# Performance work log

Hardware: AMD Instinct MI355X
Metric: run time of the kernel (lower is better)

Reference implementation:

```python
import jax, jax.numpy as jnp
import numpy as np
from jax import lax

# 4D convolution (valid padding, stride 1) via XLA's rank-general conv.
# dimension_numbers: N=batch, C=channels, then 4 spatial axes H,W,D,T.
DN = ('NCHWDT', 'OIHWDT', 'NCHWDT')

def conv4d(x, w, b):
    y = lax.conv_general_dilated(x, w, window_strides=(1, 1, 1, 1),
                                 padding='VALID', dimension_numbers=DN)
    return y + b.reshape(1, -1, 1, 1, 1, 1)


def setup_inputs() -> dict:
    key = jax.random.key(0)
    ks = jax.random.split(key, 7)
    B = 128
    x = jax.random.normal(ks[0], (B, 1, 18, 18, 18, 18), dtype=jnp.float32)
    # conv4d(1, 5, 7): weight [out=5, in=1, 7,7,7,7]
    w1 = jax.random.normal(ks[1], (5, 1, 7, 7, 7, 7), dtype=jnp.float32) * 0.02
    b1 = jax.random.normal(ks[2], (5,), dtype=jnp.float32) * 0.02
    # conv4d(5, 10, 7): weight [10, 5, 7,7,7,7]
    w2 = jax.random.normal(ks[3], (10, 5, 7, 7, 7, 7), dtype=jnp.float32) * 0.02
    b2 = jax.random.normal(ks[4], (10,), dtype=jnp.float32) * 0.02
    # Linear(10 * 6**4, 1)
    feat = 10 * 6 ** 4  # 12960
    w_lin = jax.random.normal(ks[5], (1, feat), dtype=jnp.float32) * 0.02
    b_lin = jax.random.normal(ks[6], (1,), dtype=jnp.float32) * 0.02
    return {"x": x, "w1": w1, "b1": b1, "w2": w2, "b2": b2,
            "w_lin": w_lin, "b_lin": b_lin}


def reference(x, w1, b1, w2, b2, w_lin, b_lin):
    # head: conv4d -> ReLU -> conv4d -> ReLU
    h = jax.nn.relu(conv4d(x, w1, b1))          # [B, 5, 12,12,12,12]
    h = jax.nn.relu(conv4d(h, w2, b2))          # [B, 10, 6,6,6,6]
    # out: Flatten -> Dropout(eval: identity) -> Linear -> Sigmoid
    h = h.reshape(h.shape[0], -1)               # [B, 12960]
    logits = h @ w_lin.T + b_lin                 # [B, 1]
    return jax.nn.sigmoid(logits)
```

## Files before the change

### kernel.cpp

```cpp
#include <hip/hip_runtime.h>
#include <math.h>

typedef unsigned u32;
typedef _Float16 f16x8 __attribute__((ext_vector_type(8)));
typedef float    f32x16 __attribute__((ext_vector_type(16)));

static __device__ __forceinline__ u32 pack2(_Float16 a, _Float16 b) {
    union { _Float16 h[2]; u32 u; } v;
    v.h[0] = a; v.h[1] = b;
    return v.u;
}


__global__ __launch_bounds__(256) void pack_A1p(
    const float* __restrict__ w1, _Float16* __restrict__ A1)
{
    int i = blockIdx.x * 256 + threadIdx.x;
    if (i >= 9728) return;
    u32 outv = 0u;
    int kh = i / 1164, r = i % 1164;
    if (kh < 7 && r < 1148) {
        int kw = r / 164, r2 = r % 164;
        if (r2 < 140) {
            int kd = r2 / 20, r3 = r2 % 20;
            int oc = r3 / 4, j2 = r3 % 4;
            int j0 = 2 * j2, j1 = 2 * j2 + 1;
            const float* wb = w1 + oc * 2401 + kh * 343 + kw * 49 + kd * 7;
            _Float16 v0 = (j0 < 7) ? (_Float16)wb[j0] : (_Float16)0.f;
            _Float16 v1 = (j1 < 7) ? (_Float16)wb[j1] : (_Float16)0.f;
            outv = pack2(v0, v1);
        }
    }
    ((u32*)A1)[i] = outv;
}

__global__ __launch_bounds__(256) void pack_A2p(
    const float* __restrict__ w2, _Float16* __restrict__ A2)
{
    int i = blockIdx.x * 256 + threadIdx.x;
    if (i >= 79040) return;
    int ci = i / 15808, r = i % 15808;
    int kh = r / 1976, r2 = r % 1976;
    u32 outv = 0u;
    if (kh < 7 && r2 < 1960) {
        int kw = r2 / 280, r3 = r2 % 280;
        int kd = r3 / 40, r4 = r3 % 40;
        int oc = r4 / 4, j2 = r4 % 4;
        int j0 = 2 * j2, j1 = 2 * j2 + 1;
        const float* wb = w2 + oc * 12005 + ci * 2401 + kh * 343 + kw * 49 + kd * 7;
        _Float16 v0 = (j0 < 7) ? (_Float16)wb[j0] : (_Float16)0.f;
        _Float16 v1 = (j1 < 7) ? (_Float16)wb[j1] : (_Float16)0.f;
        outv = pack2(v0, v1);
    }
    ((u32*)A2)[i] = outv;
}

#define C1_SLAB 9360
#define C1_AOFF 9360
#define C1_LDS  (9360 + 9728)
__global__ __launch_bounds__(256, 2) void conv1_mfma(
    const float* __restrict__ x, const _Float16* __restrict__ A1,
    const float* __restrict__ b1, _Float16* __restrict__ h1)
{
    __shared__ u32 lds[C1_LDS];
    int tid = threadIdx.x;
    int lane = tid & 63;
    int wave = tid >> 6;
    int col = lane & 31;
    int g = lane >> 5;

    int bid = (int)blockIdx.x;
    int lbid = (bid & 7) * 192 + (bid >> 3);
    int OWp = lbid % 3;
    int OH = (lbid / 3) & 3;
    int b = lbid / 12;

    int qn[3], u_[2], od_[2], ot_[2];
    #pragma unroll
    for (int s = 0; s < 2; ++s) {
        int nt = wave + 4 * s;
        int n = nt * 32 + col;
        int u = n / 144, r2 = n % 144;
        int od = r2 / 12, ot = r2 % 12;
        u_[s] = u; od_[s] = od; ot_[s] = ot;
        qn[s] = (u * 36 + od) * 52 + ot * 4;
    }
    {
        int r2 = 112 + col;
        int od = r2 / 12, ot = r2 % 12;
        qn[2] = (36 + od) * 52 + ot * 4;
    }

    f32x16 acc0, acc1, acc2;
    #pragma unroll
    for (int q = 0; q < 16; ++q) { acc0[q] = 0.f; acc1[q] = 0.f; acc2[q] = 0.f; }

    const float* xbase = x + (size_t)b * 104976;
    int w10 = tid / 18, id18 = tid % 18;
    int iw = 4 * OWp + w10;
    bool stager = (tid < 180);

    int mc = (col < 30) ? col : 29;
    int am_dw = mc / 15, am_dh = (mc % 15) / 5, am_oc = mc % 5;
    int jadd = 4 * (col - mc);
    int vlane = 4 * am_oc - 164 * am_dw + jadd;
    int zbase = C1_AOFF + 8312 + vlane;
    bool eLo = (am_dw == 1);
    bool e3  = (am_dw == 1) && (g == 0);
    bool e24 = (am_dw == 0) && (g == 1);
    bool eHi = (am_dw == 0);

    float2 xr[9];
    {
        const uint4* asrc = (const uint4*)A1;
        uint4* adst = (uint4*)(lds + C1_AOFF);
        #pragma unroll
        for (int i = 0; i < 10; ++i) {
            int q = tid + 256 * i;
            if (q < 2432) adst[q] = asrc[q];
        }
        if (stager) {
            const float2* src = (const float2*)(xbase + (3 * OH) * 5832 + iw * 324 + id18 * 18);
            #pragma unroll
            for (int q = 0; q < 9; ++q) xr[q] = src[q];
        }
    }

    for (int se = 0; se < 9; ++se) {
        int kh = se - am_dh;
        int vbase = (kh >= 0 && kh < 7) ? (C1_AOFF + kh * 1164 + vlane) : zbase;

        __syncthreads();
        if (stager) {
            _Float16 h[19];
            #pragma unroll
            for (int q = 0; q < 9; ++q) { h[2*q] = (_Float16)xr[q].x; h[2*q+1] = (_Float16)xr[q].y; }
            h[18] = (_Float16)0.f;
            u32 e[9], o[9];
            #pragma unroll
            for (int q = 0; q < 9; ++q) e[q] = pack2(h[2*q], h[2*q+1]);
            #pragma unroll
            for (int q = 0; q < 9; ++q) o[q] = pack2(h[2*q+1], (q < 8) ? h[2*q+2] : h[18]);
            int base = tid * 52;
            #pragma unroll
            for (int ot = 0; ot < 12; ++ot) {
                uint4 w;
                if ((ot & 1) == 0) { const int q = ot >> 1;   w = (uint4){e[q], e[q+1], e[q+2], e[q+3]}; }
                else               { const int q = (ot-1)>>1; w = (uint4){o[q], o[q+1], o[q+2], o[q+3]}; }
                *(uint4*)(&lds[base + ot * 4]) = w;
            }
        }
        __syncthreads();

        if (se < 8 && stager) {
            const float2* src = (const float2*)(xbase + (3 * OH + se + 1) * 5832 + iw * 324 + id18 * 18);
            #pragma unroll
            for (int q = 0; q < 9; ++q) xr[q] = src[q];
        }

        #pragma unroll
        for (int k2 = 0; k2 < 28; ++k2) {
            const int t0 = 2 * k2, t1 = 2 * k2 + 1;
            const int c0 = ((t0 / 7) * 18 + (t0 % 7)) * 52;
            const int c1 = ((t1 / 7) * 18 + (t1 % 7)) * 52;
            const int ca0 = 164 * (t0 / 7) + 20 * (t0 % 7);
            const int ca1 = 164 * (t1 / 7) + 20 * (t1 % 7);
            int qoff = g ? c1 : c0;
            int ca   = g ? ca1 : ca0;
            int abase;
            if (k2 <= 2)       abase = eLo ? zbase : vbase;
            else if (k2 == 3)  abase = e3  ? zbase : vbase;
            else if (k2 == 24) abase = e24 ? zbase : vbase;
            else if (k2 >= 25) abase = eHi ? zbase : vbase;
            else               abase = vbase;
            f16x8 af = *(const f16x8*)(lds + abase + ca);
            f16x8 bf0 = *(const f16x8*)(lds + qn[0] + qoff);
            f16x8 bf1 = *(const f16x8*)(lds + qn[1] + qoff);
            acc0 = __builtin_amdgcn_mfma_f32_32x32x16_f16(af, bf0, acc0, 0, 0, 0);
            acc1 = __builtin_amdgcn_mfma_f32_32x32x16_f16(af, bf1, acc1, 0, 0, 0);
            if ((k2 & 3) == wave) {
                f16x8 bf2 = *(const f16x8*)(lds + qn[2] + qoff);
                acc2 = __builtin_amdgcn_mfma_f32_32x32x16_f16(af, bf2, acc2, 0, 0, 0);
            }
        }
    }

    #pragma unroll
    for (int s = 0; s < 2; ++s) {
        f32x16 a = (s == 0) ? acc0 : acc1;
        int ow_b = 4 * OWp + 2 * u_[s];
        #pragma unroll
        for (int r = 0; r < 16; ++r) {
            const int m0 = (r & 3) + 8 * (r >> 2);
            const int m1 = m0 + 4;
            const int dw0 = m0 / 15, dh0 = (m0 % 15) / 5, oc0 = m0 % 5;
            const int dw1 = m1 / 15, dh1 = (m1 % 15) / 5, oc1 = m1 % 5;
            if (m1 >= 30 && g) continue;
            int dw = g ? dw1 : dw0;
            int dh = g ? dh1 : dh0;
            int oc = g ? oc1 : oc0;
            float bv = g ? b1[oc1] : b1[oc0];
            float v = fmaxf(a[r] + bv, 0.f);
            h1[(size_t)b * 103680 + oc * 20736 + (3 * OH + dh) * 1728
               + (ow_b + dw) * 144 + od_[s] * 12 + ot_[s]] = (_Float16)v;
        }
    }

    __syncthreads();
    {
        float* fl = (float*)lds;
        #pragma unroll
        for (int r = 0; r < 16; ++r)
            fl[wave * 1024 + r * 64 + lane] = acc2[r];
    }
    __syncthreads();
    {
        const float* fl = (const float*)lds;
        int r2 = 112 + col;
        int od = r2 / 12, ot = r2 % 12;
        int ow_b = 4 * OWp + 2;
        #pragma unroll
        for (int q = 0; q < 4; ++q) {
            int r = wave * 4 + q;
            int m = (r & 3) + 8 * (r >> 2) + 4 * g;
            if (m >= 30) continue;
            float s = fl[r * 64 + lane] + fl[1024 + r * 64 + lane]
                    + fl[2048 + r * 64 + lane] + fl[3072 + r * 64 + lane];
            int dw = m / 15, dh = (m % 15) / 5, oc = m % 5;
            float v = fmaxf(s + b1[oc], 0.f);
            h1[(size_t)b * 103680 + oc * 20736 + (3 * OH + dh) * 1728
               + (ow_b + dw) * 144 + od * 12 + ot] = (_Float16)v;
        }
    }
}

#define C2_SLAB 4032
#define C2_AOFF 4032
#define C2_LDS  (4032 + 15808)
__global__ __launch_bounds__(256, 2) void conv2_mfma(
    const _Float16* __restrict__ h1, const _Float16* __restrict__ A2,
    _Float16* __restrict__ part)
{
    __shared__ u32 lds[C2_LDS];
    int tid = threadIdx.x;
    int lane = tid & 63;
    int wave = tid >> 6;
    int col = lane & 31;
    int g = lane >> 5;

    int bid = (int)blockIdx.x;
    int lbid = (bid & 7) * 160 + (bid >> 3);
    int ci = lbid % 5;
    int OH2 = (lbid / 5) & 1;
    int b = lbid / 10;

    int qn[2], n_[2];
    #pragma unroll
    for (int s = 0; s < 2; ++s) {
        int nt = wave + 4 * s;
        int n = nt * 32 + col;
        n_[s] = n;
        int nc = (n < 216) ? n : 215;
        int ow = nc / 36, rem = nc % 36;
        int od = rem / 6, ot = rem % 6;
        qn[s] = (ow * 12 + od) * 28 + ot * 4;
    }

    f32x16 acc0, acc1;
    #pragma unroll
    for (int q = 0; q < 16; ++q) { acc0[q] = 0.f; acc1[q] = 0.f; }

    const _Float16* hbase = h1 + (size_t)b * 103680 + ci * 20736;
    int iw = tid / 12, id12 = tid % 12;
    bool stager = (tid < 144);

    int mc = (col < 30) ? col : 29;
    int am_dh = mc / 10, am_oc = mc % 10;
    int jadd = 4 * (col - mc);
    int vlane = 4 * am_oc + jadd;
    int zb = C2_AOFF + 13832 + vlane;

    uint2 xr[3];
    {
        const uint4* asrc = (const uint4*)A2 + (size_t)ci * 3952;
        uint4* adst = (uint4*)(lds + C2_AOFF);
        #pragma unroll
        for (int i = 0; i < 16; ++i) {
            int q = tid + 256 * i;
            if (q < 3952) adst[q] = asrc[q];
        }
        if (stager) {
            const uint2* src = (const uint2*)(hbase + (3 * OH2) * 1728 + iw * 144 + id12 * 12);
            #pragma unroll
            for (int q = 0; q < 3; ++q) xr[q] = src[q];
        }
    }

    for (int she = 0; she < 9; ++she) {
        int kh = she - am_dh;
        int vb = (kh >= 0 && kh < 7) ? (C2_AOFF + kh * 1976 + vlane) : zb;

        __syncthreads();
        if (stager) {
            _Float16 h[14];
            *(uint2*)&h[0] = xr[0]; *(uint2*)&h[4] = xr[1]; *(uint2*)&h[8] = xr[2];
            h[12] = (_Float16)0.f;
            u32 e[6], o[6];
            #pragma unroll
            for (int q = 0; q < 6; ++q) e[q] = pack2(h[2*q], h[2*q+1]);
            #pragma unroll
            for (int q = 0; q < 6; ++q) o[q] = pack2(h[2*q+1], (q < 5) ? h[2*q+2] : h[12]);
            int base = tid * 28;
            #pragma unroll
            for (int ot = 0; ot < 6; ++ot) {
                uint4 w;
                if ((ot & 1) == 0) { const int q = ot >> 1;   w = (uint4){e[q], e[q+1], e[q+2], e[q+3]}; }
                else               { const int q = (ot-1)>>1; w = (uint4){o[q], o[q+1], o[q+2], o[q+3]}; }
                *(uint4*)(&lds[base + ot * 4]) = w;
            }
        }
        __syncthreads();

        if (she < 8 && stager) {
            const uint2* src = (const uint2*)(hbase + (3 * OH2 + she + 1) * 1728 + iw * 144 + id12 * 12);
            #pragma unroll
            for (int q = 0; q < 3; ++q) xr[q] = src[q];
        }

        #pragma unroll
        for (int k2 = 0; k2 < 25; ++k2) {
            const int t0 = 2 * k2, t1 = 2 * k2 + 1;
            const int c0 = ((t0 / 7) * 12 + (t0 % 7)) * 28;
            const int c1 = (t1 < 49) ? ((t1 / 7) * 12 + (t1 % 7)) * 28 : 0;
            const int a0 = 280 * (t0 / 7) + 40 * (t0 % 7);
            const int a1 = (t1 < 49) ? (280 * (t1 / 7) + 40 * (t1 % 7)) : 0;
            int qoff = g ? c1 : c0;
            int ca   = g ? a1 : a0;
            int ab = (k2 == 24 && g) ? zb : vb;
            f16x8 af = *(const f16x8*)(lds + ab + ca);
            f16x8 bf0 = *(const f16x8*)(lds + qn[0] + qoff);
            acc0 = __builtin_amdgcn_mfma_f32_32x32x16_f16(af, bf0, acc0, 0, 0, 0);
            if (wave < 3) {
                f16x8 bf1 = *(const f16x8*)(lds + qn[1] + qoff);
                acc1 = __builtin_amdgcn_mfma_f32_32x32x16_f16(af, bf1, acc1, 0, 0, 0);
            }
        }
    }

    #pragma unroll
    for (int s = 0; s < 2; ++s) {
        if (s == 1 && wave >= 3) continue;
        if (n_[s] >= 216) continue;
        f32x16 a = (s == 0) ? acc0 : acc1;
        #pragma unroll
        for (int r = 0; r < 16; ++r) {
            const int m0 = (r & 3) + 8 * (r >> 2);
            const int m1 = m0 + 4;
            const int dh0 = m0 / 10, oc0 = m0 % 10;
            const int dh1 = m1 / 10, oc1 = m1 % 10;
            if (m1 >= 30 && g) continue;
            int dh = g ? dh1 : dh0;
            int oc = g ? oc1 : oc0;
            int oh = 3 * OH2 + dh;
            part[((size_t)(ci * 768 + b * 6 + oh) * 10 + oc) * 216 + n_[s]] = (_Float16)a[r];
        }
    }
}

__global__ __launch_bounds__(256) void out_fused(
    const _Float16* __restrict__ part, const float* __restrict__ b2,
    const float* __restrict__ wl, const float* __restrict__ bl,
    float* __restrict__ out)
{
    int b = blockIdx.x;
    int tid = threadIdx.x;
    float s = 0.f;
    for (int i = tid; i < 12960; i += 256) {
        int oc = i / 1296;
        int rem = i % 1296;
        int oh = rem / 216;
        int n = rem % 216;
        float v = 0.f;
        #pragma unroll
        for (int ci = 0; ci < 5; ++ci)
            v += (float)part[((size_t)(ci * 768 + b * 6 + oh) * 10 + oc) * 216 + n];
        v = fmaxf(v + b2[oc], 0.f);
        s += v * wl[i];
    }
    #pragma unroll
    for (int off = 32; off > 0; off >>= 1)
        s += __shfl_down(s, off, 64);
    __shared__ float wsum[4];
    int wave = tid >> 6;
    if ((tid & 63) == 0) wsum[wave] = s;
    __syncthreads();
    if (tid == 0) {
        float tot = wsum[0] + wsum[1] + wsum[2] + wsum[3] + bl[0];
        out[b] = 1.f / (1.f + expf(-tot));
    }
}

extern "C" void kernel_launch(void* const* d_in, const int* in_sizes, int n_in,
                              void* d_out, int out_size, void* d_ws, size_t ws_size,
                              hipStream_t stream) {
    const float* x  = (const float*)d_in[0];
    const float* w1 = (const float*)d_in[1];
    const float* b1 = (const float*)d_in[2];
    const float* w2 = (const float*)d_in[3];
    const float* b2 = (const float*)d_in[4];
    const float* wl = (const float*)d_in[5];
    const float* bl = (const float*)d_in[6];
    float* out = (float*)d_out;

    _Float16* h1   = (_Float16*)d_ws;
    _Float16* A1   = h1 + 13271040;
    _Float16* A2   = A1 + 129024;
    _Float16* part = A2 + 576000;

    pack_A1p<<<38, 256, 0, stream>>>(w1, A1);
    pack_A2p<<<309, 256, 0, stream>>>(w2, A2);
    conv1_mfma<<<1536, 256, 0, stream>>>(x, A1, b1, h1);
    conv2_mfma<<<1280, 256, 0, stream>>>(h1, A2, part);
    out_fused<<<128, 256, 0, stream>>>(part, b2, wl, bl, out);
}
```

Measured before the change: 232.9 us.

## Balance conv2 MFMA work across waves by splitting remaining N-tiles along K

In conv2_mfma, waves 0-2 previously handled two 32-column N tiles while wave 3 handled one, leaving the load uneven. Now each wave owns one full tile, and the three leftover tiles are split along the reduction (k2) dimension round-robin across all four waves. The partial accumulators are reduced through LDS after a barrier. This evens out MFMA issue per wave, at the cost of three extra accumulator registers sets (register pressure at 2 blocks/SM), an LDS round trip and two extra syncs.

Result: slower. 244.7 us (+5.1%).

```diff
diff --git a/kernel.cpp b/kernel.cpp
--- a/kernel.cpp
+++ b/kernel.cpp
@@ -254,21 +254,25 @@
     int OH2 = (lbid / 5) & 1;
     int b = lbid / 10;
 
-    int qn[2], n_[2];
-    #pragma unroll
-    for (int s = 0; s < 2; ++s) {
-        int nt = wave + 4 * s;
-        int n = nt * 32 + col;
-        n_[s] = n;
+    int qnF, qnR[3];
+    {
+        int n = wave * 32 + col;
+        int ow = n / 36, rem = n % 36;
+        int od = rem / 6, ot = rem % 6;
+        qnF = (ow * 12 + od) * 28 + ot * 4;
+    }
+    #pragma unroll
+    for (int t = 0; t < 3; ++t) {
+        int n = (4 + t) * 32 + col;
         int nc = (n < 216) ? n : 215;
         int ow = nc / 36, rem = nc % 36;
         int od = rem / 6, ot = rem % 6;
-        qn[s] = (ow * 12 + od) * 28 + ot * 4;
-    }
-
-    f32x16 acc0, acc1;
-    #pragma unroll
-    for (int q = 0; q < 16; ++q) { acc0[q] = 0.f; acc1[q] = 0.f; }
+        qnR[t] = (ow * 12 + od) * 28 + ot * 4;
+    }
+
+    f32x16 accF, accR0, accR1, accR2;
+    #pragma unroll
+    for (int q = 0; q < 16; ++q) { accF[q] = 0.f; accR0[q] = 0.f; accR1[q] = 0.f; accR2[q] = 0.f; }
 
     const _Float16* hbase = h1 + (size_t)b * 103680 + ci * 20736;
     int iw = tid / 12, id12 = tid % 12;
@@ -338,31 +342,67 @@
             int ca   = g ? a1 : a0;
             int ab = (k2 == 24 && g) ? zb : vb;
             f16x8 af = *(const f16x8*)(lds + ab + ca);
-            f16x8 bf0 = *(const f16x8*)(lds + qn[0] + qoff);
-            acc0 = __builtin_amdgcn_mfma_f32_32x32x16_f16(af, bf0, acc0, 0, 0, 0);
-            if (wave < 3) {
-                f16x8 bf1 = *(const f16x8*)(lds + qn[1] + qoff);
-                acc1 = __builtin_amdgcn_mfma_f32_32x32x16_f16(af, bf1, acc1, 0, 0, 0);
-            }
-        }
-    }
-
-    #pragma unroll
-    for (int s = 0; s < 2; ++s) {
-        if (s == 1 && wave >= 3) continue;
-        if (n_[s] >= 216) continue;
-        f32x16 a = (s == 0) ? acc0 : acc1;
+            f16x8 bfF = *(const f16x8*)(lds + qnF + qoff);
+            accF = __builtin_amdgcn_mfma_f32_32x32x16_f16(af, bfF, accF, 0, 0, 0);
+            if (((k2 + 0) & 3) == wave) {
+                f16x8 bf = *(const f16x8*)(lds + qnR[0] + qoff);
+                accR0 = __builtin_amdgcn_mfma_f32_32x32x16_f16(af, bf, accR0, 0, 0, 0);
+            }
+            if (((k2 + 1) & 3) == wave) {
+                f16x8 bf = *(const f16x8*)(lds + qnR[1] + qoff);
+                accR1 = __builtin_amdgcn_mfma_f32_32x32x16_f16(af, bf, accR1, 0, 0, 0);
+            }
+            if (((k2 + 2) & 3) == wave) {
+                f16x8 bf = *(const f16x8*)(lds + qnR[2] + qoff);
+                accR2 = __builtin_amdgcn_mfma_f32_32x32x16_f16(af, bf, accR2, 0, 0, 0);
+            }
+        }
+    }
+
+    {
+        int n = wave * 32 + col;
         #pragma unroll
         for (int r = 0; r < 16; ++r) {
             const int m0 = (r & 3) + 8 * (r >> 2);
             const int m1 = m0 + 4;
-            const int dh0 = m0 / 10, oc0 = m0 % 10;
-            const int dh1 = m1 / 10, oc1 = m1 % 10;
             if (m1 >= 30 && g) continue;
-            int dh = g ? dh1 : dh0;
-            int oc = g ? oc1 : oc0;
+            int m = g ? m1 : m0;
+            int dh = m / 10, oc = m % 10;
             int oh = 3 * OH2 + dh;
-            part[((size_t)(ci * 768 + b * 6 + oh) * 10 + oc) * 216 + n_[s]] = (_Float16)a[r];
+            part[((size_t)(ci * 768 + b * 6 + oh) * 10 + oc) * 216 + n] = (_Float16)accF[r];
+        }
+    }
+
+    __syncthreads();
+    {
+        float* fl = (float*)lds;
+        #pragma unroll
+        for (int r = 0; r < 16; ++r) fl[        wave * 1024 + r * 64 + lane] = accR0[r];
+        #pragma unroll
+        for (int r = 0; r < 16; ++r) fl[4096 +  wave * 1024 + r * 64 + lane] = accR1[r];
+        #pragma unroll
+        for (int r = 0; r < 16; ++r) fl[8192 +  wave * 1024 + r * 64 + lane] = accR2[r];
+    }
+    __syncthreads();
+    {
+        const float* fl = (const float*)lds;
+        #pragma unroll
+        for (int t = 0; t < 3; ++t) {
+            int n = (4 + t) * 32 + col;
+            if (n >= 216) continue;
+            #pragma unroll
+            for (int q = 0; q < 4; ++q) {
+                int r = wave * 4 + q;
+                int m = (r & 3) + 8 * (r >> 2) + 4 * g;
+                if (m >= 30) continue;
+                float s = fl[t * 4096 + r * 64 + lane]
+                        + fl[t * 4096 + 1024 + r * 64 + lane]
+                        + fl[t * 4096 + 2048 + r * 64 + lane]
+                        + fl[t * 4096 + 3072 + r * 64 + lane];
+                int dh = m / 10, oc = m % 10;
+                int oh = 3 * OH2 + dh;
+                part[((size_t)(ci * 768 + b * 6 + oh) * 10 + oc) * 216 + n] = (_Float16)s;
+            }
         }
     }
 }
```
